# Kernel tuning notes

Measured on AMD Instinct MI355X. Metric: run time of the kernel, lower is better.

Reference implementation:

```python
import jax, jax.numpy as jnp
from jax import lax
import numpy as np

TAU = 2.0      # LIF membrane time constant
VTH = 1.0      # spikingjelly LIFNode default v_threshold
ALPHA = 2.0    # spikingjelly surrogate.ATan default alpha

# Heaviside spike with ATan surrogate gradient (spikingjelly semantics)
@jax.custom_vjp
def spike(x):
    return (x >= 0.0).astype(x.dtype)

def _spike_fwd(x):
    return spike(x), x

def _spike_bwd(x, g):
    sg = (ALPHA / 2.0) / (1.0 + (jnp.pi / 2.0 * ALPHA * x) ** 2)
    return (g * sg,)

spike.defvjp(_spike_fwd, _spike_bwd)

def lif_step(v, x):
    # decay_input=True, v_reset=0.0, hard reset (spikingjelly LIFNode defaults)
    v = v + (x - v) / TAU
    s = spike(v - VTH)
    v = v * (1.0 - s)
    return v, s

def conv1d_same(x, k):
    # x: [N, L], k: [K]  -> depthwise-style 1D conv with SAME padding
    y = lax.conv_general_dilated(x[:, None, :], k[None, None, :], (1,), 'SAME')
    return y[:, 0, :]

def setup_inputs() -> dict:
    key = jax.random.key(0)
    ks = jax.random.split(key, 16)
    N, T, D, C, NC = 4096, 16, 700, 128, 20
    def lin(kw, kb, fout, fin):
        s = 1.0 / np.sqrt(fin)
        W = jax.random.uniform(kw, (fout, fin), jnp.float32, -s, s)
        b = jax.random.uniform(kb, (fout,), jnp.float32, -s, s)
        return W, b
    x = jax.random.normal(ks[0], (N, T, D), jnp.float32)
    W_in, b_in = lin(ks[1], ks[2], C, D)
    W_rec, b_rec = lin(ks[3], ks[4], C, C)
    W2, b2 = lin(ks[5], ks[6], C, C)
    k_t = jax.random.normal(ks[7], (3,), jnp.float32) * 0.5   # TATCA temporal conv, kernel_size_t=3
    k_c = jax.random.normal(ks[8], (3,), jnp.float32) * 0.5   # TATCA channel conv
    W_p, b_p = lin(ks[9], ks[10], C, C)
    W_out, b_out = lin(ks[11], ks[12], NC, C)
    return {"x": x, "W_in": W_in, "b_in": b_in, "W_rec": W_rec, "b_rec": b_rec,
            "W2": W2, "b2": b2, "k_t": k_t, "k_c": k_c,
            "W_p": W_p, "b_p": b_p, "W_out": W_out, "b_out": b_out}

def reference(x, W_in, b_in, W_rec, b_rec, W2, b2, k_t, k_c, W_p, b_p, W_out, b_out):
    N, T, D = x.shape
    C = W_in.shape[0]
    z = jnp.zeros((N, C), x.dtype)

    def step(carry, frame):
        v1, v2, spikes_last = carry
        inp = frame @ W_in.T + b_in + spikes_last @ W_rec.T + b_rec
        v1, s1 = lif_step(v1, inp)
        x2 = s1 @ W2.T + b2
        v2, feat = lif_step(v2, x2)
        return (v1, v2, s1), feat

    xs = jnp.transpose(x, (1, 0, 2))          # [T, N, D]
    _, features = lax.scan(step, (z, z, z), xs)  # [T, N, C]

    # TATCA_1D: temporal attention (conv over T, kernel 3) x channel attention (conv over C)
    t_att = jax.nn.sigmoid(conv1d_same(features.mean(2).T, k_t)).T   # [T, N]
    c_att = jax.nn.sigmoid(conv1d_same(features.mean(0), k_c))       # [N, C]
    attended = features * t_att[:, :, None] * c_att[None, :, :]

    def step2(v3, feat):
        h = feat @ W_p.T + b_p
        v3, s = lif_step(v3, h)
        return v3, s @ W_out.T + b_out

    _, outs = lax.scan(step2, z, attended)    # [T, N, num_classes]
    return outs.mean(0), features, attended
```

## Files before the change

### kernel.cpp

```cpp
#include <hip/hip_runtime.h>
#include <hip/hip_bf16.h>
#include <stdint.h>


typedef __attribute__((ext_vector_type(8))) _Float16 half8;
typedef __attribute__((ext_vector_type(4))) float f32x4;
typedef unsigned long long u64;

#define MFMA16F(a, b, c) __builtin_amdgcn_mfma_f32_16x16x32_f16(a, b, c, 0, 0, 0)

__device__ inline void gload16(const void* g, void* l) {
  __builtin_amdgcn_global_load_lds(
      (const __attribute__((address_space(1))) uint32_t*)g,
      (__attribute__((address_space(3))) uint32_t*)l, 16, 0, 0);
}

__device__ inline void splitf16(float4 q0, float4 q1, half8& hh, half8& ll) {
  float f[8] = {q0.x, q0.y, q0.z, q0.w, q1.x, q1.y, q1.z, q1.w};
  _Float16 H[8], L[8];
#pragma unroll
  for (int j = 0; j < 8; ++j) {
    _Float16 h1 = (_Float16)(f[j] * 16.0f);
    float r = fmaf((float)h1, -0.0625f, f[j]);
    L[j] = (_Float16)(r * 32768.0f);
    H[j] = h1;
  }
  __builtin_memcpy(&hh, H, 16);
  __builtin_memcpy(&ll, L, 16);
}

__global__ void k_prep(const float* __restrict__ Wr, const float* __restrict__ W2,
                       const float* __restrict__ Wp, const float* __restrict__ Win,
                       float* __restrict__ WrT, float* __restrict__ W2T,
                       float* __restrict__ WpT, ushort* __restrict__ F2) {
  int idx = blockIdx.x * blockDim.x + threadIdx.x;
  if (idx < 3 * 16384) {
    int sel = idx >> 14;
    int r = idx & 16383;
    int j = r >> 7, c = r & 127;
    const float* src = (sel == 0) ? Wr : (sel == 1) ? W2 : Wp;
    float* dst = (sel == 0) ? WrT : (sel == 1) ? W2T : WpT;
    dst[r] = src[c * 128 + j];
  } else {
    int i2 = idx - 49152;
    if (i2 >= 128 * 704) return;
    int c = i2 / 704, d = i2 - c * 704;
    float w = (d < 700) ? Win[c * 700 + d] : 0.f;
    _Float16 b1 = (_Float16)(w * 256.0f);
    float r = fmaf((float)b1, -0.00390625f, w);
    _Float16 b2 = (_Float16)(r * 524288.0f);
    ushort u1, u2;
    __builtin_memcpy(&u1, &b1, 2);
    __builtin_memcpy(&u2, &b2, 2);
    F2[i2] = u1;
    F2[90112 + i2] = u2;
  }
}

__global__ __launch_bounds__(512, 4) void k_gemm_scan(
    const float* __restrict__ x, const ushort* __restrict__ F2,
    const float* __restrict__ b_in, const float* __restrict__ b_rec,
    const float* __restrict__ WrT, const float* __restrict__ W2T,
    const float* __restrict__ b2, const float* __restrict__ WpT,
    const float* __restrict__ b_p, const float* __restrict__ W_out,
    const float* __restrict__ b_out, const float* __restrict__ k_t,
    const float* __restrict__ k_c, float* __restrict__ features,
    float* __restrict__ attended, float* __restrict__ out0) {
  __shared__ __align__(16) char lds[81920];

  const int tid = threadIdx.x;
  const int w = tid >> 6;
  const int l = tid & 63;
  const int blk = blockIdx.x;
  const int wr = w >> 2;
  const int wc = w & 3;

  const int jA = (((l & 7) ^ (l >> 3)) * 4);
  int arow[2];
#pragma unroll
  for (int i = 0; i < 2; ++i)
    arow[i] = (blk * 128 + (w * 2 + i) * 8 + (l >> 3)) * 700;
  const ushort* bsrc[2];
  int bdst[2];
#pragma unroll
  for (int i = 0; i < 2; ++i) {
    int idx = w * 2 + i;
    int plane = idx >> 3, cg = idx & 7;
    int col = cg * 16 + (l >> 2);
    bsrc[i] = F2 + plane * 90112 + col * 704 + (((l & 3) ^ ((l >> 3) & 3)) * 8);
    bdst[i] = 16384 + plane * 8192 + cg * 1024;
  }
  const int adst = (w * 2) * 1024;

  const int lm = l & 15, kh = l >> 4;
  const int p0 = ((2 * kh) ^ (lm & 7)) * 16;
  const int p1 = ((2 * kh + 1) ^ (lm & 7)) * 16;
  const int bswz = (kh ^ ((lm >> 1) & 3)) * 16;
  int aoff[4], boff[2];
#pragma unroll
  for (int mf = 0; mf < 4; ++mf) aoff[mf] = (wr * 64 + mf * 16 + lm) * 128;
#pragma unroll
  for (int nf = 0; nf < 2; ++nf) boff[nf] = 16384 + (wc * 32 + nf * 16 + lm) * 64 + bswz;

  f32x4 acc_h[4][2], acc_m[4][2];
#pragma unroll
  for (int i = 0; i < 4; ++i)
#pragma unroll
    for (int j = 0; j < 2; ++j) {
      acc_h[i][j] = (f32x4){0.f, 0.f, 0.f, 0.f};
      acc_m[i][j] = (f32x4){0.f, 0.f, 0.f, 0.f};
    }

  auto STAGE = [&](int buf, int kt) {
    const int k0 = kt * 32;
    char* base = lds + buf * 32768;
#pragma unroll
    for (int i = 0; i < 2; ++i) {
      int k = k0 + jA;
      int off = (k < 700) ? (arow[i] + k) : 0;
      gload16(x + off, base + adst + i * 1024);
    }
#pragma unroll
    for (int i = 0; i < 2; ++i)
      gload16(bsrc[i] + k0, base + bdst[i]);
  };

  STAGE(0, 0);
  __syncthreads();
  int buf = 0;
  for (int kt = 0; kt < 22; ++kt) {
    if (kt + 1 < 22) STAGE(buf ^ 1, kt + 1);
    const char* base = lds + buf * 32768;
    half8 b1[2], b2f[2];
#pragma unroll
    for (int nf = 0; nf < 2; ++nf) {
      const char* bb = base + boff[nf];
      b1[nf] = *(const half8*)(bb);
      b2f[nf] = *(const half8*)(bb + 8192);
    }
#pragma unroll
    for (int mf = 0; mf < 4; ++mf) {
      const char* ab = base + aoff[mf];
      float4 q0 = *(const float4*)(ab + p0);
      float4 q1 = *(const float4*)(ab + p1);
      half8 a1, a2;
      splitf16(q0, q1, a1, a2);
#pragma unroll
      for (int nf = 0; nf < 2; ++nf) {
        acc_h[mf][nf] = MFMA16F(a1, b1[nf], acc_h[mf][nf]);
        acc_m[mf][nf] = MFMA16F(a1, b2f[nf], acc_m[mf][nf]);
        acc_m[mf][nf] = MFMA16F(a2, b1[nf], acc_m[mf][nf]);
      }
    }
    __syncthreads();
    buf ^= 1;
  }

  float* XWs = (float*)lds;
#pragma unroll
  for (int nf = 0; nf < 2; ++nf) {
    int col = wc * 32 + nf * 16 + lm;
    float bias = b_in[col] + b_rec[col];
    int colx = col ^ (kh << 3);
#pragma unroll
    for (int mf = 0; mf < 4; ++mf) {
      int rowl = wr * 64 + mf * 16 + kh * 4;
#pragma unroll
      for (int r = 0; r < 4; ++r)
        XWs[(rowl + r) * 128 + colx] =
            acc_h[mf][nf][r] * 0.000244140625f +
            acc_m[mf][nf][r] * 1.1920928955078125e-7f + bias;
    }
  }
  __syncthreads();

  const int s = w;
  const int n_glob = blk * 8 + s;
  char* sc = lds + 65536 + s * 2048;
  u64* fmaskp = (u64*)sc;
  float* tap = (float*)(sc + 256);
  float* cap = (float*)(sc + 320);
  float* gp = (float*)(sc + 832);

  const float b2a = b2[l], b2b = b2[l + 64];
  float v1a = 0.f, v1b = 0.f, v2a = 0.f, v2b = 0.f, fsa = 0.f, fsb = 0.f;
  u64 pm0 = 0ull, pm1 = 0ull;

  for (int t = 0; t < 16; ++t) {
    const float* xrow = XWs + (s * 16 + t) * 128;
    const int key = ((t >> 2) & 3) << 3;
    float ia = xrow[l ^ key];
    float ib = xrow[(l + 64) ^ key];
    u64 q0 = pm0, q1 = pm1;
    while (q0) { int j = __builtin_ctzll(q0); q0 &= q0 - 1;
      ia += WrT[j * 128 + l]; ib += WrT[j * 128 + l + 64]; }
    while (q1) { int j = __builtin_ctzll(q1); q1 &= q1 - 1;
      ia += WrT[(64 + j) * 128 + l]; ib += WrT[(64 + j) * 128 + l + 64]; }
    v1a = v1a + (ia - v1a) * 0.5f;
    bool sa = (v1a - 1.0f) >= 0.f; v1a = sa ? 0.f : v1a;
    v1b = v1b + (ib - v1b) * 0.5f;
    bool sb = (v1b - 1.0f) >= 0.f; v1b = sb ? 0.f : v1b;
    pm0 = __ballot((int)sa);
    pm1 = __ballot((int)sb);
    float xa = b2a, xb = b2b;
    u64 r0 = pm0, r1 = pm1;
    while (r0) { int j = __builtin_ctzll(r0); r0 &= r0 - 1;
      xa += W2T[j * 128 + l]; xb += W2T[j * 128 + l + 64]; }
    while (r1) { int j = __builtin_ctzll(r1); r1 &= r1 - 1;
      xa += W2T[(64 + j) * 128 + l]; xb += W2T[(64 + j) * 128 + l + 64]; }
    v2a = v2a + (xa - v2a) * 0.5f;
    bool fa = (v2a - 1.0f) >= 0.f; v2a = fa ? 0.f : v2a;
    v2b = v2b + (xb - v2b) * 0.5f;
    bool fb = (v2b - 1.0f) >= 0.f; v2b = fb ? 0.f : v2b;
    float ffa = fa ? 1.f : 0.f, ffb = fb ? 1.f : 0.f;
    features[(size_t)((t << 12) | n_glob) * 128 + l] = ffa;
    features[(size_t)((t << 12) | n_glob) * 128 + l + 64] = ffb;
    fsa += ffa; fsb += ffb;
    u64 f0 = __ballot((int)fa), f1 = __ballot((int)fb);
    if (l == 0) { fmaskp[t * 2 + 0] = f0; fmaskp[t * 2 + 1] = f1; }
  }

  gp[l] = fsa * (1.f / 16.f);
  gp[l + 64] = fsb * (1.f / 16.f);

  if (l < 16) {
    float acc = 0.f;
#pragma unroll
    for (int j = 0; j < 3; ++j) {
      int tt = l - 1 + j;
      if (tt >= 0 && tt < 16) {
        float m = (float)(__popcll(fmaskp[tt * 2 + 0]) +
                          __popcll(fmaskp[tt * 2 + 1])) * (1.f / 128.f);
        acc += k_t[j] * m;
      }
    }
    tap[l] = 1.f / (1.f + expf(-acc));
  }
  {
    float mm1 = (l == 0) ? 0.f : gp[l - 1];
    float acc = k_c[0] * mm1 + k_c[1] * gp[l] + k_c[2] * gp[l + 1];
    cap[l] = 1.f / (1.f + expf(-acc));
    float np1 = (l == 63) ? 0.f : gp[l + 65];
    float acc2 = k_c[0] * gp[l + 63] + k_c[1] * gp[l + 64] + k_c[2] * np1;
    cap[l + 64] = 1.f / (1.f + expf(-acc2));
  }

  const float bpa = b_p[l], bpb = b_p[l + 64];
  const float caa = cap[l], cab = cap[l + 64];
  float v3a = 0.f, v3b = 0.f, ssa = 0.f, ssb = 0.f;
  for (int t = 0; t < 16; ++t) {
    u64 m0 = fmaskp[t * 2 + 0], m1 = fmaskp[t * 2 + 1];
    float tat = tap[t];
    bool ba = (m0 >> l) & 1, bb = (m1 >> l) & 1;
    attended[(size_t)((t << 12) | n_glob) * 128 + l] = ba ? tat * caa : 0.f;
    attended[(size_t)((t << 12) | n_glob) * 128 + l + 64] = bb ? tat * cab : 0.f;
    float ha = bpa, hb = bpb;
    u64 q0 = m0, q1 = m1;
    while (q0) { int j = __builtin_ctzll(q0); q0 &= q0 - 1;
      float w_ = tat * cap[j];
      ha += w_ * WpT[j * 128 + l]; hb += w_ * WpT[j * 128 + l + 64]; }
    while (q1) { int j = __builtin_ctzll(q1); q1 &= q1 - 1;
      float w_ = tat * cap[64 + j];
      ha += w_ * WpT[(64 + j) * 128 + l]; hb += w_ * WpT[(64 + j) * 128 + l + 64]; }
    v3a = v3a + (ha - v3a) * 0.5f;
    bool sa = (v3a - 1.0f) >= 0.f; v3a = sa ? 0.f : v3a;
    ssa += sa ? 1.f : 0.f;
    v3b = v3b + (hb - v3b) * 0.5f;
    bool sb = (v3b - 1.0f) >= 0.f; v3b = sb ? 0.f : v3b;
    ssb += sb ? 1.f : 0.f;
  }
  gp[l] = ssa * (1.f / 16.f);
  gp[l + 64] = ssb * (1.f / 16.f);
  if (l < 20) {
    float acc = b_out[l];
    for (int j = 0; j < 128; ++j) acc += gp[j] * W_out[l * 128 + j];
    out0[n_glob * 20 + l] = acc;
  }
}

extern "C" void kernel_launch(void* const* d_in, const int* in_sizes, int n_in,
                              void* d_out, int out_size, void* d_ws, size_t ws_size,
                              hipStream_t stream) {
  const float* x     = (const float*)d_in[0];
  const float* W_in  = (const float*)d_in[1];
  const float* b_in  = (const float*)d_in[2];
  const float* W_rec = (const float*)d_in[3];
  const float* b_rec = (const float*)d_in[4];
  const float* W2    = (const float*)d_in[5];
  const float* b2    = (const float*)d_in[6];
  const float* k_t   = (const float*)d_in[7];
  const float* k_c   = (const float*)d_in[8];
  const float* W_p   = (const float*)d_in[9];
  const float* b_p   = (const float*)d_in[10];
  const float* W_out = (const float*)d_in[11];
  const float* b_out = (const float*)d_in[12];

  float* out      = (float*)d_out;
  float* out0     = out;
  float* features = out + 81920;
  float* attended = out + 81920 + 8388608;

  float* ws  = (float*)d_ws;
  float* WrT = ws;
  float* W2T = ws + 16384;
  float* WpT = ws + 32768;
  ushort* F2 = (ushort*)(ws + 49152);

  hipLaunchKernelGGL(k_prep, dim3(544), dim3(256), 0, stream,
                     W_rec, W2, W_p, W_in, WrT, W2T, WpT, F2);
  hipLaunchKernelGGL(k_gemm_scan, dim3(512), dim3(512), 0, stream,
                     x, F2, b_in, b_rec, WrT, W2T, b2, WpT, b_p, W_out, b_out,
                     k_t, k_c, features, attended, out0);
}
```

Measured before the change: 78.60 us.

## Shrink GEMM tile to 64 rows per block and load x directly to registers

Each block now covers 4 samples (64 rows) with 256 threads instead of 8 samples with 512, and the grid doubles to 1024 blocks. The x operand is no longer staged through LDS. Each wave reads its 16 rows straight from global memory into registers, prefetching one k-step ahead, and runs all 8 N-fragments against a shared B tile. LDS use falls from 80KB to about 39KB, which allows more resident blocks per CU. The XW scratch uses a padded stride of 130 instead of an XOR swizzle, and the sync between the XW store and the scan was dropped. That is safe only because each wave reads back only the rows it wrote itself. The trade-off is uncoalesced row-wise global loads of x and more B-tile reloads across blocks.

```diff
diff --git a/kernel.cpp b/kernel.cpp
--- a/kernel.cpp
+++ b/kernel.cpp
@@ -57,7 +57,7 @@
   }
 }
 
-__global__ __launch_bounds__(512, 4) void k_gemm_scan(
+__global__ __launch_bounds__(256, 4) void k_gemm_scan(
     const float* __restrict__ x, const ushort* __restrict__ F2,
     const float* __restrict__ b_in, const float* __restrict__ b_rec,
     const float* __restrict__ WrT, const float* __restrict__ W2T,
@@ -66,117 +66,94 @@
     const float* __restrict__ b_out, const float* __restrict__ k_t,
     const float* __restrict__ k_c, float* __restrict__ features,
     float* __restrict__ attended, float* __restrict__ out0) {
-  __shared__ __align__(16) char lds[81920];
+  __shared__ __align__(16) char lds[39424];
 
   const int tid = threadIdx.x;
   const int w = tid >> 6;
   const int l = tid & 63;
   const int blk = blockIdx.x;
-  const int wr = w >> 2;
-  const int wc = w & 3;
-
-  const int jA = (((l & 7) ^ (l >> 3)) * 4);
-  int arow[2];
-#pragma unroll
-  for (int i = 0; i < 2; ++i)
-    arow[i] = (blk * 128 + (w * 2 + i) * 8 + (l >> 3)) * 700;
-  const ushort* bsrc[2];
-  int bdst[2];
-#pragma unroll
-  for (int i = 0; i < 2; ++i) {
-    int idx = w * 2 + i;
+  const int lm = l & 15, kh = l >> 4;
+
+  const float* xr = x + (size_t)(blk * 64 + w * 16 + lm) * 700;
+
+  const ushort* bsrc[4];
+  int bdst[4];
+#pragma unroll
+  for (int i = 0; i < 4; ++i) {
+    int idx = w * 4 + i;
     int plane = idx >> 3, cg = idx & 7;
     int col = cg * 16 + (l >> 2);
     bsrc[i] = F2 + plane * 90112 + col * 704 + (((l & 3) ^ ((l >> 3) & 3)) * 8);
-    bdst[i] = 16384 + plane * 8192 + cg * 1024;
-  }
-  const int adst = (w * 2) * 1024;
-
-  const int lm = l & 15, kh = l >> 4;
-  const int p0 = ((2 * kh) ^ (lm & 7)) * 16;
-  const int p1 = ((2 * kh + 1) ^ (lm & 7)) * 16;
-  const int bswz = (kh ^ ((lm >> 1) & 3)) * 16;
-  int aoff[4], boff[2];
-#pragma unroll
-  for (int mf = 0; mf < 4; ++mf) aoff[mf] = (wr * 64 + mf * 16 + lm) * 128;
-#pragma unroll
-  for (int nf = 0; nf < 2; ++nf) boff[nf] = 16384 + (wc * 32 + nf * 16 + lm) * 64 + bswz;
-
-  f32x4 acc_h[4][2], acc_m[4][2];
-#pragma unroll
-  for (int i = 0; i < 4; ++i)
-#pragma unroll
-    for (int j = 0; j < 2; ++j) {
-      acc_h[i][j] = (f32x4){0.f, 0.f, 0.f, 0.f};
-      acc_m[i][j] = (f32x4){0.f, 0.f, 0.f, 0.f};
-    }
+    bdst[i] = plane * 8192 + cg * 1024;
+  }
+  const int bkey = (lm >> 1) & 3;
+  const int brd = lm * 64 + ((kh ^ bkey) * 16);
+
+  f32x4 acc_h[8], acc_m[8];
+#pragma unroll
+  for (int j = 0; j < 8; ++j) {
+    acc_h[j] = (f32x4){0.f, 0.f, 0.f, 0.f};
+    acc_m[j] = (f32x4){0.f, 0.f, 0.f, 0.f};
+  }
 
   auto STAGE = [&](int buf, int kt) {
     const int k0 = kt * 32;
-    char* base = lds + buf * 32768;
-#pragma unroll
-    for (int i = 0; i < 2; ++i) {
-      int k = k0 + jA;
-      int off = (k < 700) ? (arow[i] + k) : 0;
-      gload16(x + off, base + adst + i * 1024);
-    }
-#pragma unroll
-    for (int i = 0; i < 2; ++i)
-      gload16(bsrc[i] + k0, base + bdst[i]);
+#pragma unroll
+    for (int i = 0; i < 4; ++i)
+      gload16(bsrc[i] + k0, lds + buf * 16384 + bdst[i]);
   };
+  auto LOADA = [&](int kt, float4& q0, float4& q1) {
+    const int k0 = kt * 32 + kh * 8;
+    q0 = *(const float4*)(xr + k0);
+    if (kt == 21 && kh == 3)
+      q1 = make_float4(0.f, 0.f, 0.f, 0.f);
+    else
+      q1 = *(const float4*)(xr + k0 + 4);
+  };
 
   STAGE(0, 0);
+  float4 qa, qb;
+  LOADA(0, qa, qb);
   __syncthreads();
   int buf = 0;
   for (int kt = 0; kt < 22; ++kt) {
-    if (kt + 1 < 22) STAGE(buf ^ 1, kt + 1);
-    const char* base = lds + buf * 32768;
-    half8 b1[2], b2f[2];
-#pragma unroll
-    for (int nf = 0; nf < 2; ++nf) {
-      const char* bb = base + boff[nf];
-      b1[nf] = *(const half8*)(bb);
-      b2f[nf] = *(const half8*)(bb + 8192);
+    float4 na = {}, nb = {};
+    if (kt < 21) {
+      STAGE(buf ^ 1, kt + 1);
+      LOADA(kt + 1, na, nb);
     }
-#pragma unroll
-    for (int mf = 0; mf < 4; ++mf) {
-      const char* ab = base + aoff[mf];
-      float4 q0 = *(const float4*)(ab + p0);
-      float4 q1 = *(const float4*)(ab + p1);
-      half8 a1, a2;
-      splitf16(q0, q1, a1, a2);
-#pragma unroll
-      for (int nf = 0; nf < 2; ++nf) {
-        acc_h[mf][nf] = MFMA16F(a1, b1[nf], acc_h[mf][nf]);
-        acc_m[mf][nf] = MFMA16F(a1, b2f[nf], acc_m[mf][nf]);
-        acc_m[mf][nf] = MFMA16F(a2, b1[nf], acc_m[mf][nf]);
-      }
+    half8 a1, a2;
+    splitf16(qa, qb, a1, a2);
+    const char* bb0 = lds + buf * 16384 + brd;
+#pragma unroll
+    for (int nf = 0; nf < 8; ++nf) {
+      const char* bb = bb0 + nf * 1024;
+      half8 b1 = *(const half8*)(bb);
+      half8 b2f = *(const half8*)(bb + 8192);
+      acc_h[nf] = MFMA16F(a1, b1, acc_h[nf]);
+      acc_m[nf] = MFMA16F(a1, b2f, acc_m[nf]);
+      acc_m[nf] = MFMA16F(a2, b1, acc_m[nf]);
     }
     __syncthreads();
+    qa = na; qb = nb;
     buf ^= 1;
   }
 
   float* XWs = (float*)lds;
 #pragma unroll
-  for (int nf = 0; nf < 2; ++nf) {
-    int col = wc * 32 + nf * 16 + lm;
-    float bias = b_in[col] + b_rec[col];
-    int colx = col ^ (kh << 3);
-#pragma unroll
-    for (int mf = 0; mf < 4; ++mf) {
-      int rowl = wr * 64 + mf * 16 + kh * 4;
-#pragma unroll
-      for (int r = 0; r < 4; ++r)
-        XWs[(rowl + r) * 128 + colx] =
-            acc_h[mf][nf][r] * 0.000244140625f +
-            acc_m[mf][nf][r] * 1.1920928955078125e-7f + bias;
-    }
-  }
-  __syncthreads();
-
-  const int s = w;
-  const int n_glob = blk * 8 + s;
-  char* sc = lds + 65536 + s * 2048;
+  for (int nf = 0; nf < 8; ++nf) {
+    const int col = nf * 16 + lm;
+    const float bias = b_in[col] + b_rec[col];
+    const int rowb = w * 16 + kh * 4;
+#pragma unroll
+    for (int r = 0; r < 4; ++r)
+      XWs[(rowb + r) * 130 + col] =
+          acc_h[nf][r] * 0.000244140625f +
+          acc_m[nf][r] * 1.1920928955078125e-7f + bias;
+  }
+
+  const int n_glob = blk * 4 + w;
+  char* sc = lds + 33280 + w * 1536;
   u64* fmaskp = (u64*)sc;
   float* tap = (float*)(sc + 256);
   float* cap = (float*)(sc + 320);
@@ -187,10 +164,9 @@
   u64 pm0 = 0ull, pm1 = 0ull;
 
   for (int t = 0; t < 16; ++t) {
-    const float* xrow = XWs + (s * 16 + t) * 128;
-    const int key = ((t >> 2) & 3) << 3;
-    float ia = xrow[l ^ key];
-    float ib = xrow[(l + 64) ^ key];
+    const float* xrow = XWs + (w * 16 + t) * 130;
+    float ia = xrow[l];
+    float ib = xrow[l + 64];
     u64 q0 = pm0, q1 = pm1;
     while (q0) { int j = __builtin_ctzll(q0); q0 &= q0 - 1;
       ia += WrT[j * 128 + l]; ib += WrT[j * 128 + l + 64]; }
@@ -308,7 +284,7 @@
 
   hipLaunchKernelGGL(k_prep, dim3(544), dim3(256), 0, stream,
                      W_rec, W2, W_p, W_in, WrT, W2T, WpT, F2);
-  hipLaunchKernelGGL(k_gemm_scan, dim3(512), dim3(512), 0, stream,
+  hipLaunchKernelGGL(k_gemm_scan, dim3(1024), dim3(256), 0, stream,
                      x, F2, b_in, b_rec, WrT, W2T, b2, WpT, b_p, W_out, b_out,
                      k_t, k_c, features, attended, out0);
 }
```

Result: faster. 74.69 us (-5.0%).
